# Performance work log

Hardware: AMD Instinct MI355X
Metric: run time of the kernel (lower is better)

## Reference

```python
import jax, jax.numpy as jnp
import numpy as np

NUM_ROWS = 1_000_000
NUM_COLS = 1_000_000
NNZ = 32_000_000


def setup_inputs() -> dict:
    key = jax.random.key(0)
    k_sx, k_x, k_sel, k_ro = jax.random.split(key, 4)
    sx = jax.random.normal(k_sx, (NNZ,), dtype=jnp.float32)
    x = jax.random.normal(k_x, (NUM_COLS,), dtype=jnp.float32)
    selector_idx = jax.random.randint(k_sel, (NNZ,), 0, NUM_COLS, dtype=jnp.int32)
    # CSR row pointers: ro[0]=0, ro[-1]=NNZ, interior sorted random split points
    interior = jnp.sort(jax.random.randint(k_ro, (NUM_ROWS - 1,), 0, NNZ, dtype=jnp.int32))
    row_end_offsets = jnp.concatenate([
        jnp.zeros((1,), jnp.int32), interior, jnp.full((1,), NNZ, jnp.int32)
    ])
    y = jnp.zeros((NUM_ROWS,), dtype=jnp.float32)
    return {"sx": sx, "x": x, "y": y,
            "selector_idx": selector_idx, "row_end_offsets": row_end_offsets}


def reference(sx, x, y, selector_idx, row_end_offsets):
    # CSR SpMV: y[r] = sum_{j in [ro[r], ro[r+1])} sx[j] * x[selector_idx[j]]
    nnz = sx.shape[0]
    num_rows = row_end_offsets.shape[0] - 1
    # map each nonzero j to its row id (handles empty rows correctly)
    row_ids = jnp.searchsorted(row_end_offsets, jnp.arange(nnz, dtype=jnp.int32),
                               side="right") - 1
    prod = sx * x[selector_idx]            # gather + multiply, [nnz]
    out = jax.ops.segment_sum(prod, row_ids, num_segments=num_rows)  # [num_rows]
    return out
```

## Files before the change

### kernel.cpp

```cpp
#include <hip/hip_runtime.h>


constexpr int ITEMS     = 16;
constexpr int BLOCK     = 256;
constexpr int CHUNK_NNZ = BLOCK * ITEMS;
constexpr int SRO_CAP   = 4098;

typedef float f32x4 __attribute__((ext_vector_type(4)));
typedef int   i32x4 __attribute__((ext_vector_type(4)));

__global__ __launch_bounds__(256) void zero_out(float* __restrict__ y, int n) {
    int i = blockIdx.x * blockDim.x + threadIdx.x;
    if (i < n) y[i] = 0.0f;
}

__device__ __forceinline__ int row_of(const int* __restrict__ ro,
                                      int num_rows, int key) {
    int left = 1, right = num_rows;
    while (left < right) {
        int mid = (left + right) >> 1;
        if (ro[mid] <= key) left = mid + 1; else right = mid;
    }
    return left - 1;
}

__global__ __launch_bounds__(BLOCK) void spmv_chunk(
    const float* __restrict__ sx,
    const float* __restrict__ x,
    const int*   __restrict__ sel,
    const int*   __restrict__ ro,
    float*       __restrict__ y,
    int nnz, int num_rows)
{
    __shared__ int sro[SRO_CAP];
    __shared__ int s_lo, s_hi;

    const int b  = blockIdx.x;
    const int B0 = b * CHUNK_NNZ;
    const int B1 = min(nnz, B0 + CHUNK_NNZ);

    if (threadIdx.x == 0)         s_lo = row_of(ro, num_rows, B0);
    if (threadIdx.x == BLOCK - 1) s_hi = row_of(ro, num_rows, B1 - 1);
    __syncthreads();

    const int lo = s_lo;
    const int n  = s_hi + 2 - lo;
    const bool use_lds = (n <= SRO_CAP);
    if (use_lds) {
        for (int i = threadIdx.x; i < n; i += BLOCK) sro[i] = ro[lo + i];
    }
    __syncthreads();

    const int j0 = (b * BLOCK + threadIdx.x) * ITEMS;
    if (j0 >= nnz) return;
    const int j1 = min(nnz, j0 + ITEMS);

    float sum = 0.0f;

    if (use_lds && j1 - j0 == ITEMS) {
        int left = 1, right = n - 1;
        while (left < right) {
            int mid = (left + right) >> 1;
            if (sro[mid] <= j0) left = mid + 1; else right = mid;
        }
        int r_local  = left - 1;
        int row_end  = sro[r_local + 1];

        f32x4 s[ITEMS / 4];
        i32x4 c[ITEMS / 4];
        #pragma unroll
        for (int v = 0; v < ITEMS / 4; ++v) {
            s[v] = __builtin_nontemporal_load(
                       reinterpret_cast<const f32x4*>(sx + j0) + v);
            c[v] = __builtin_nontemporal_load(
                       reinterpret_cast<const i32x4*>(sel + j0) + v);
        }
        float p[ITEMS];
        #pragma unroll
        for (int v = 0; v < ITEMS / 4; ++v) {
            #pragma unroll
            for (int k = 0; k < 4; ++k) {
                p[v * 4 + k] = s[v][k] * x[c[v][k]];
            }
        }

        #pragma unroll
        for (int k = 0; k < ITEMS; ++k) {
            int jj = j0 + k;
            while (jj >= row_end) {
                if (sum != 0.0f) atomicAdd(&y[lo + r_local], sum);
                sum = 0.0f;
                ++r_local;
                row_end = sro[r_local + 1];
            }
            sum += p[k];
        }
        if (sum != 0.0f) atomicAdd(&y[lo + r_local], sum);
    } else {
        int r       = row_of(ro, num_rows, j0);
        int row_end = ro[r + 1];
        for (int j = j0; j < j1; ++j) {
            while (j >= row_end) {
                if (sum != 0.0f) atomicAdd(&y[r], sum);
                sum = 0.0f;
                ++r;
                row_end = ro[r + 1];
            }
            sum += sx[j] * x[sel[j]];
        }
        if (sum != 0.0f) atomicAdd(&y[r], sum);
    }
}

extern "C" void kernel_launch(void* const* d_in, const int* in_sizes, int n_in,
                              void* d_out, int out_size, void* d_ws, size_t ws_size,
                              hipStream_t stream) {
    const float* sx  = (const float*)d_in[0];
    const float* x   = (const float*)d_in[1];
    const int*   sel = (const int*)d_in[3];
    const int*   ro  = (const int*)d_in[4];
    float*       y   = (float*)d_out;

    const int nnz      = in_sizes[0];
    const int num_rows = in_sizes[4] - 1;

    {
        int threads = 256;
        int blocks  = (out_size + threads - 1) / threads;
        zero_out<<<blocks, threads, 0, stream>>>(y, out_size);
    }
    {
        int blocks = (nnz + CHUNK_NNZ - 1) / CHUNK_NNZ;
        spmv_chunk<<<blocks, BLOCK, 0, stream>>>(sx, x, sel, ro, y, nnz, num_rows);
    }
}
```

Baseline: 257.8 us.

## Gather x values directly into LDS via global_load_lds instead of registers

Replaces the per-thread register gather of x[sel[j]] with asynchronous global_load_lds instructions that write each gathered value into a per-wave LDS slab, followed by a block barrier before the multiply-accumulate. The intent is to raise memory-level parallelism and lower VGPR pressure during the random gather. It also shrinks the cached row-pointer LDS buffer so the new slab fits, which sends more chunks with many short rows to the slow global fallback path. The tail-chunk handling changes too: full-width vector loads are now issued for a partially filled last chunk.

After: 273.3 us. 1.06x slower.

```diff
diff --git a/kernel.cpp b/kernel.cpp
--- a/kernel.cpp
+++ b/kernel.cpp
@@ -3,11 +3,19 @@
 
 constexpr int ITEMS     = 16;
 constexpr int BLOCK     = 256;
+constexpr int WAVES     = BLOCK / 64;
 constexpr int CHUNK_NNZ = BLOCK * ITEMS;
-constexpr int SRO_CAP   = 4098;
+constexpr int SRO_CAP   = 1536;
 
 typedef float f32x4 __attribute__((ext_vector_type(4)));
 typedef int   i32x4 __attribute__((ext_vector_type(4)));
+
+__device__ __forceinline__ void gather_to_lds(const float* g, void* lds) {
+    __builtin_amdgcn_global_load_lds(
+        (const __attribute__((address_space(1))) void*)g,
+        (__attribute__((address_space(3))) void*)lds,
+        4, 0, 0);
+}
 
 __global__ __launch_bounds__(256) void zero_out(float* __restrict__ y, int n) {
     int i = blockIdx.x * blockDim.x + threadIdx.x;
@@ -32,8 +40,12 @@
     float*       __restrict__ y,
     int nnz, int num_rows)
 {
-    __shared__ int sro[SRO_CAP];
-    __shared__ int s_lo, s_hi;
+    __shared__ int   sro[SRO_CAP];
+    __shared__ float slab[WAVES][ITEMS][64];
+    __shared__ int   s_lo, s_hi;
+
+    const int lane = threadIdx.x & 63;
+    const int wid  = threadIdx.x >> 6;
 
     const int b  = blockIdx.x;
     const int B0 = b * CHUNK_NNZ;
@@ -51,55 +63,64 @@
     }
     __syncthreads();
 
-    const int j0 = (b * BLOCK + threadIdx.x) * ITEMS;
-    if (j0 >= nnz) return;
-    const int j1 = min(nnz, j0 + ITEMS);
+    const int  j0     = (b * BLOCK + threadIdx.x) * ITEMS;
+    const bool active = (j0 < nnz);
 
-    float sum = 0.0f;
+    if (use_lds) {
+        int r_local = 0, row_end = 0;
+        f32x4 s[ITEMS / 4];
 
-    if (use_lds && j1 - j0 == ITEMS) {
-        int left = 1, right = n - 1;
-        while (left < right) {
-            int mid = (left + right) >> 1;
-            if (sro[mid] <= j0) left = mid + 1; else right = mid;
-        }
-        int r_local  = left - 1;
-        int row_end  = sro[r_local + 1];
+        if (active) {
+            int left = 1, right = n - 1;
+            while (left < right) {
+                int mid = (left + right) >> 1;
+                if (sro[mid] <= j0) left = mid + 1; else right = mid;
+            }
+            r_local = left - 1;
+            row_end = sro[r_local + 1];
 
-        f32x4 s[ITEMS / 4];
-        i32x4 c[ITEMS / 4];
-        #pragma unroll
-        for (int v = 0; v < ITEMS / 4; ++v) {
-            s[v] = __builtin_nontemporal_load(
-                       reinterpret_cast<const f32x4*>(sx + j0) + v);
-            c[v] = __builtin_nontemporal_load(
-                       reinterpret_cast<const i32x4*>(sel + j0) + v);
-        }
-        float p[ITEMS];
-        #pragma unroll
-        for (int v = 0; v < ITEMS / 4; ++v) {
+            i32x4 c[ITEMS / 4];
             #pragma unroll
-            for (int k = 0; k < 4; ++k) {
-                p[v * 4 + k] = s[v][k] * x[c[v][k]];
+            for (int v = 0; v < ITEMS / 4; ++v) {
+                c[v] = __builtin_nontemporal_load(
+                           reinterpret_cast<const i32x4*>(sel + j0) + v);
+            }
+            #pragma unroll
+            for (int v = 0; v < ITEMS / 4; ++v) {
+                #pragma unroll
+                for (int k = 0; k < 4; ++k) {
+                    gather_to_lds(x + c[v][k], &slab[wid][v * 4 + k][0]);
+                }
+            }
+            #pragma unroll
+            for (int v = 0; v < ITEMS / 4; ++v) {
+                s[v] = __builtin_nontemporal_load(
+                           reinterpret_cast<const f32x4*>(sx + j0) + v);
             }
         }
 
-        #pragma unroll
-        for (int k = 0; k < ITEMS; ++k) {
-            int jj = j0 + k;
-            while (jj >= row_end) {
-                if (sum != 0.0f) atomicAdd(&y[lo + r_local], sum);
-                sum = 0.0f;
-                ++r_local;
-                row_end = sro[r_local + 1];
+        __syncthreads();
+
+        if (active) {
+            float sum = 0.0f;
+            #pragma unroll
+            for (int k = 0; k < ITEMS; ++k) {
+                int jj = j0 + k;
+                while (jj >= row_end) {
+                    if (sum != 0.0f) atomicAdd(&y[lo + r_local], sum);
+                    sum = 0.0f;
+                    ++r_local;
+                    row_end = sro[r_local + 1];
+                }
+                sum += slab[wid][k][lane] * s[k >> 2][k & 3];
             }
-            sum += p[k];
+            if (sum != 0.0f) atomicAdd(&y[lo + r_local], sum);
         }
-        if (sum != 0.0f) atomicAdd(&y[lo + r_local], sum);
-    } else {
+    } else if (active) {
         int r       = row_of(ro, num_rows, j0);
         int row_end = ro[r + 1];
-        for (int j = j0; j < j1; ++j) {
+        float sum = 0.0f;
+        for (int j = j0; j < min(nnz, j0 + ITEMS); ++j) {
             while (j >= row_end) {
                 if (sum != 0.0f) atomicAdd(&y[r], sum);
                 sum = 0.0f;
```
